# Kernel optimization log

Hardware: AMD Instinct MI355X
Metric: run time of the kernel (lower is better)

The kernel has to match this reference:

```python
import jax, jax.numpy as jnp
import numpy as np

B, C, HZ, WZ, HX, WX = 128, 256, 8, 8, 32, 32
NC = HZ * WZ              # correlation channels = num_channel = 64
TC = max(8, NC // 32)     # CoordAttention bottleneck channels = 8
EPS = 1e-5


def setup_inputs() -> dict:
    key = jax.random.key(0)
    ks = jax.random.split(key, 8)
    z = jax.random.normal(ks[0], (B, C, HZ, WZ), dtype=jnp.float32)
    x = jax.random.normal(ks[1], (B, C, HX, WX), dtype=jnp.float32)
    # 1x1 conv weights stored as [out, in]
    conv1_w = jax.random.normal(ks[2], (TC, NC), dtype=jnp.float32) * (1.0 / np.sqrt(NC))
    conv1_b = jnp.zeros((TC,), dtype=jnp.float32)
    bn_gamma = jnp.ones((TC,), dtype=jnp.float32)
    bn_beta = jnp.zeros((TC,), dtype=jnp.float32)
    conv2_w = jax.random.normal(ks[3], (NC, TC), dtype=jnp.float32) * (1.0 / np.sqrt(TC))
    conv2_b = jnp.zeros((NC,), dtype=jnp.float32)
    conv3_w = jax.random.normal(ks[4], (NC, TC), dtype=jnp.float32) * (1.0 / np.sqrt(TC))
    conv3_b = jnp.zeros((NC,), dtype=jnp.float32)
    return dict(z=z, x=x, conv1_w=conv1_w, conv1_b=conv1_b, bn_gamma=bn_gamma,
                bn_beta=bn_beta, conv2_w=conv2_w, conv2_b=conv2_b,
                conv3_w=conv3_w, conv3_b=conv3_b)


def _h_swish(v):
    return v * jnp.clip(v + 3.0, 0.0, 6.0) / 6.0  # x * relu6(x+3)/6


def reference(z, x, conv1_w, conv1_b, bn_gamma, bn_beta, conv2_w, conv2_b, conv3_w, conv3_b):
    b, c, H, W = x.shape
    # pixel-wise correlation (per-sample loop == batched matmul): [b, Hz*Wz, H, W]
    corr = jnp.einsum('bck,bcn->bkn', z.reshape(b, c, -1), x.reshape(b, c, -1))
    corr = corr.reshape(b, -1, H, W)
    # CoordAttention
    x_h = corr.mean(axis=3)                       # pool over W -> [b, NC, H]
    x_w = corr.mean(axis=2)                       # pool over H -> [b, NC, W]
    x_cat = jnp.concatenate([x_h, x_w], axis=2)   # [b, NC, H+W]
    y = jnp.einsum('oc,bcl->bol', conv1_w, x_cat) + conv1_b[None, :, None]
    # BatchNorm2d (training-mode batch statistics, biased variance)
    mu = y.mean(axis=(0, 2), keepdims=True)
    var = y.var(axis=(0, 2), keepdims=True)
    y = (y - mu) * jax.lax.rsqrt(var + EPS) * bn_gamma[None, :, None] + bn_beta[None, :, None]
    y = _h_swish(y)
    yh, yw = y[:, :, :H], y[:, :, H:]
    out_h = jax.nn.sigmoid(jnp.einsum('oc,bcl->bol', conv2_w, yh) + conv2_b[None, :, None])  # [b, NC, H]
    out_w = jax.nn.sigmoid(jnp.einsum('oc,bcl->bol', conv3_w, yw) + conv3_b[None, :, None])  # [b, NC, W]
    return corr * out_w[:, :, None, :] * out_h[:, :, :, None]
```

## Files before the change

kernel.cpp:

```cpp
#include <hip/hip_runtime.h>
#include <hip/hip_bf16.h>
#include <math.h>

#define B_   128
#define C_   256
#define K_   64
#define N_   1024
#define H_   32
#define W_   32
#define TC_  8
#define L_   64
#define EPS_ 1e-5f

__global__ __launch_bounds__(256) void kA_corr(const float* __restrict__ z,
                                               const float* __restrict__ x,
                                               float* __restrict__ corr,
                                               float* __restrict__ xcat)
{
    __shared__ float zs[64 * 64];
    __shared__ float xs[64 * 64];

    const int t   = blockIdx.x;
    const int b   = blockIdx.y;
    const int tid = threadIdx.x;
    const int tk  = tid & 15;
    const int tn  = tid >> 4;
    const int k0  = tk * 4;
    const int n0  = tn * 4;

    const float* zb = z + (size_t)b * C_ * K_;
    const float* xb = x + (size_t)b * C_ * N_ + t * 64;

    float acc[4][4] = {};

    for (int cc = 0; cc < C_; cc += 64) {
        #pragma unroll
        for (int i = 0; i < 4; ++i) {
            int f4  = tid + i * 256;
            int row = f4 >> 4;
            int col = (f4 & 15) << 2;
            *(float4*)&zs[row * 64 + col] =
                *(const float4*)&zb[(size_t)(cc + row) * K_ + col];
            *(float4*)&xs[row * 64 + col] =
                *(const float4*)&xb[(size_t)(cc + row) * N_ + col];
        }
        __syncthreads();

        #pragma unroll 8
        for (int c = 0; c < 64; ++c) {
            float4 zv = *(float4*)&zs[c * 64 + k0];
            float4 xv = *(float4*)&xs[c * 64 + n0];
            float za[4] = {zv.x, zv.y, zv.z, zv.w};
            float xa[4] = {xv.x, xv.y, xv.z, xv.w};
            #pragma unroll
            for (int i = 0; i < 4; ++i)
                #pragma unroll
                for (int j = 0; j < 4; ++j)
                    acc[i][j] = fmaf(za[i], xa[j], acc[i][j]);
        }
        __syncthreads();
    }

    float* cb = corr + (size_t)b * K_ * N_ + t * 64;
    #pragma unroll
    for (int i = 0; i < 4; ++i) {
        float4 v = make_float4(acc[i][0], acc[i][1], acc[i][2], acc[i][3]);
        *(float4*)&cb[(size_t)(k0 + i) * N_ + n0] = v;
    }

    float* pw = zs;
    float* ph = zs + 2048;

    float rs[4];
    #pragma unroll
    for (int i = 0; i < 4; ++i)
        rs[i] = acc[i][0] + acc[i][1] + acc[i][2] + acc[i][3];
    #pragma unroll
    for (int i = 0; i < 4; ++i)
        ph[(k0 + i) * 16 + tn] = rs[i];

    if (tn < 8) {
        #pragma unroll
        for (int i = 0; i < 4; ++i)
            #pragma unroll
            for (int j = 0; j < 4; ++j)
                pw[(k0 + i) * 32 + n0 + j] = acc[i][j];
    }
    __syncthreads();
    if (tn >= 8) {
        #pragma unroll
        for (int i = 0; i < 4; ++i)
            #pragma unroll
            for (int j = 0; j < 4; ++j)
                pw[(k0 + i) * 32 + (n0 - 32) + j] += acc[i][j];
    }
    __syncthreads();

    float* xcb = xcat + (size_t)b * K_ * L_;
    if (tid < 128) {
        int k = tid >> 1, hl = tid & 1;
        float s = 0.f;
        #pragma unroll
        for (int q = 0; q < 8; ++q) s += ph[k * 16 + hl * 8 + q];
        xcb[k * L_ + 2 * t + hl] = s * (1.f / 32.f);
    }
    #pragma unroll
    for (int r = 0; r < 8; ++r) {
        int idx = tid + r * 256;
        int k = idx >> 5, w = idx & 31;
        atomicAdd(&xcb[k * L_ + 32 + w], pw[k * 32 + w] * (1.f / 32.f));
    }
}

__global__ __launch_bounds__(256) void kB_conv1(const float* __restrict__ xcat,
                                                const float* __restrict__ w1,
                                                const float* __restrict__ b1,
                                                float* __restrict__ ypre,
                                                float* __restrict__ stats)
{
    __shared__ float xc[64 * 64];
    __shared__ float w1s[TC_ * 64];
    __shared__ float ys[TC_ * 64];

    const int b   = blockIdx.x;
    const int tid = threadIdx.x;
    const float* xcb = xcat + (size_t)b * K_ * L_;

    #pragma unroll
    for (int i = 0; i < 4; ++i) {
        int f4 = tid + i * 256;
        *(float4*)&xc[f4 * 4] = *(const float4*)&xcb[f4 * 4];
    }
    if (tid < 128) *(float4*)&w1s[tid * 4] = *(const float4*)&w1[tid * 4];
    __syncthreads();

    const int o0 = tid >> 6;
    const int l  = tid & 63;
    float y0 = 0.f, y1 = 0.f;
    #pragma unroll 8
    for (int k = 0; k < 64; ++k) {
        float xv = xc[k * 64 + l];
        y0 = fmaf(w1s[o0 * 64 + k],        xv, y0);
        y1 = fmaf(w1s[(o0 + 4) * 64 + k],  xv, y1);
    }
    y0 += b1[o0];
    y1 += b1[o0 + 4];
    ypre[((size_t)b * TC_ + o0)     * L_ + l] = y0;
    ypre[((size_t)b * TC_ + o0 + 4) * L_ + l] = y1;
    ys[o0 * L_ + l]       = y0;
    ys[(o0 + 4) * L_ + l] = y1;
    __syncthreads();

    if (tid < TC_) {
        float s = 0.f, sq = 0.f;
        for (int q = 0; q < L_; ++q) {
            float v = ys[tid * L_ + q];
            s += v;
            sq = fmaf(v, v, sq);
        }
        atomicAdd(&stats[tid],       s);
        atomicAdd(&stats[TC_ + tid], sq);
    }
}

__global__ __launch_bounds__(256) void kD_gate(const float* __restrict__ ypre,
                                               const float* __restrict__ stats,
                                               const float* __restrict__ gamma,
                                               const float* __restrict__ beta,
                                               const float* __restrict__ w2,
                                               const float* __restrict__ b2,
                                               const float* __restrict__ w3,
                                               const float* __restrict__ b3,
                                               float* __restrict__ outh,
                                               float* __restrict__ outw)
{
    __shared__ float yn[TC_ * L_];
    __shared__ float w2s[K_ * TC_];
    __shared__ float w3s[K_ * TC_];
    __shared__ float b2s[K_], b3s[K_];

    const int b   = blockIdx.x;
    const int tid = threadIdx.x;
    const float inv_n = 1.f / (float)(B_ * L_);

    #pragma unroll
    for (int r = 0; r < 2; ++r) {
        int idx = tid + r * 256;
        int o   = idx >> 6;
        float mu  = stats[o] * inv_n;
        float var = stats[TC_ + o] * inv_n - mu * mu;
        float v = ypre[(size_t)b * TC_ * L_ + idx];
        v = (v - mu) * (1.f / sqrtf(var + EPS_)) * gamma[o] + beta[o];
        v = v * fminf(fmaxf(v + 3.f, 0.f), 6.f) * (1.f / 6.f);
        yn[idx] = v;
    }
    if (tid < 128)      *(float4*)&w2s[tid * 4]         = *(const float4*)&w2[tid * 4];
    else                *(float4*)&w3s[(tid - 128) * 4] = *(const float4*)&w3[(tid - 128) * 4];
    if (tid < 64)       b2s[tid]       = b2[tid];
    else if (tid < 128) b3s[tid - 64]  = b3[tid - 64];
    __syncthreads();

    #pragma unroll
    for (int r = 0; r < 16; ++r) {
        int idx   = tid + r * 256;
        int which = idx >> 11;
        int o     = (idx >> 5) & 63;
        int p     = idx & 31;
        const float* wsm = which ? w3s : w2s;
        const float* bsm = which ? b3s : b2s;
        float s = bsm[o];
        #pragma unroll
        for (int tt = 0; tt < TC_; ++tt)
            s = fmaf(wsm[o * TC_ + tt], yn[tt * L_ + which * H_ + p], s);
        s = 1.f / (1.f + __expf(-s));
        float* dst = which ? outw : outh;
        dst[((size_t)b * K_ + o) * H_ + p] = s;
    }
}

__global__ __launch_bounds__(256) void kE_final(float* __restrict__ out,
                                                const float* __restrict__ outh,
                                                const float* __restrict__ outw)
{
    int idx = blockIdx.x * 256 + threadIdx.x;
    int w4 = idx & 7;
    int h  = (idx >> 3) & 31;
    int bk = idx >> 8;
    float4 c4 = ((const float4*)out)[idx];
    float  oh = outh[bk * H_ + h];
    float4 ow = *(const float4*)&outw[bk * H_ + w4 * 4];
    c4.x *= ow.x * oh;
    c4.y *= ow.y * oh;
    c4.z *= ow.z * oh;
    c4.w *= ow.w * oh;
    ((float4*)out)[idx] = c4;
}

extern "C" void kernel_launch(void* const* d_in, const int* in_sizes, int n_in,
                              void* d_out, int out_size, void* d_ws, size_t ws_size,
                              hipStream_t stream)
{
    const float* z     = (const float*)d_in[0];
    const float* x     = (const float*)d_in[1];
    const float* w1    = (const float*)d_in[2];
    const float* b1    = (const float*)d_in[3];
    const float* gamma = (const float*)d_in[4];
    const float* beta  = (const float*)d_in[5];
    const float* w2    = (const float*)d_in[6];
    const float* b2    = (const float*)d_in[7];
    const float* w3    = (const float*)d_in[8];
    const float* b3    = (const float*)d_in[9];
    float* out = (float*)d_out;
    float* ws  = (float*)d_ws;

    float* xcat  = ws;
    float* stats = ws + 524288;
    float* ypre  = ws + 524304;
    float* outh  = ws + 589840;
    float* outw  = ws + 852  - 0 + 851984 - 852;
    outw = ws + 851984;

    hipMemsetAsync(ws, 0, (size_t)(524288 + 16) * sizeof(float), stream);

    kA_corr <<<dim3(16, B_), 256, 0, stream>>>(z, x, out, xcat);
    kB_conv1<<<B_,          256, 0, stream>>>(xcat, w1, b1, ypre, stats);
    kD_gate <<<B_,          256, 0, stream>>>(ypre, stats, gamma, beta,
                                              w2, b2, w3, b3, outh, outw);
    kE_final<<<(B_ * K_ * N_) / (256 * 4), 256, 0, stream>>>(out, outh, outw);
}
```

Measured before the change: 268.5 us.

## Retile correlation GEMM to 64x512 blocks with async double-buffered LDS loads

```diff
diff --git a/kernel.cpp b/kernel.cpp
--- a/kernel.cpp
+++ b/kernel.cpp
@@ -12,103 +12,141 @@
 #define L_   64
 #define EPS_ 1e-5f
 
-__global__ __launch_bounds__(256) void kA_corr(const float* __restrict__ z,
-                                               const float* __restrict__ x,
-                                               float* __restrict__ corr,
-                                               float* __restrict__ xcat)
-{
-    __shared__ float zs[64 * 64];
-    __shared__ float xs[64 * 64];
-
-    const int t   = blockIdx.x;
-    const int b   = blockIdx.y;
-    const int tid = threadIdx.x;
-    const int tk  = tid & 15;
-    const int tn  = tid >> 4;
-    const int k0  = tk * 4;
-    const int n0  = tn * 4;
+typedef __attribute__((address_space(3))) void       as3_void;
+typedef const __attribute__((address_space(1))) void as1_void;
+
+__device__ __forceinline__ void gload16(const float* g, float* lds) {
+    __builtin_amdgcn_global_load_lds((as1_void*)g, (as3_void*)lds, 16, 0, 0);
+}
+
+__global__ __launch_bounds__(256, 1) void kA_corr(const float* __restrict__ z,
+                                                  const float* __restrict__ x,
+                                                  float* __restrict__ corr,
+                                                  float* __restrict__ xcat)
+{
+    __shared__ float zs[2][32][64];
+    __shared__ float xs[2][32][512];
+
+    const int nt   = blockIdx.x;
+    const int b    = blockIdx.y;
+    const int tid  = threadIdx.x;
+    const int wv   = tid >> 6;
+    const int lane = tid & 63;
+    const int tk   = tid >> 5;
+    const int tn   = tid & 31;
 
     const float* zb = z + (size_t)b * C_ * K_;
-    const float* xb = x + (size_t)b * C_ * N_ + t * 64;
-
-    float acc[4][4] = {};
-
-    for (int cc = 0; cc < C_; cc += 64) {
-        #pragma unroll
-        for (int i = 0; i < 4; ++i) {
-            int f4  = tid + i * 256;
-            int row = f4 >> 4;
-            int col = (f4 & 15) << 2;
-            *(float4*)&zs[row * 64 + col] =
-                *(const float4*)&zb[(size_t)(cc + row) * K_ + col];
-            *(float4*)&xs[row * 64 + col] =
-                *(const float4*)&xb[(size_t)(cc + row) * N_ + col];
-        }
+    const float* xb = x + (size_t)b * C_ * N_ + nt * 512;
+
+    int sx[4];
+    #pragma unroll
+    for (int r = 0; r < 4; ++r) {
+        int s = tn * 4 + r;
+        sx[r] = s ^ ((s >> 3) & 7);
+    }
+
+    float acc[8][16] = {};
+
+    auto stage = [&](int buf, int cs) {
+        const int cc = cs * 32;
+        #pragma unroll
+        for (int q = 0; q < 18; ++q) {
+            int ch = wv + 4 * q;
+            if (ch < 8) {
+                int row = ch * 4 + (lane >> 4);
+                int col = (lane & 15) * 4;
+                gload16(zb + (size_t)(cc + row) * K_ + col, &zs[buf][ch * 4][0]);
+            } else {
+                int xc  = ch - 8;
+                int qf  = xc * 64 + lane;
+                int row = qf >> 7;
+                int sp  = qf & 127;
+                int sl  = sp ^ ((sp >> 3) & 7);
+                gload16(xb + (size_t)(cc + row) * N_ + sl * 4,
+                        &xs[buf][0][0] + xc * 256);
+            }
+        }
+    };
+
+    stage(0, 0);
+    asm volatile("s_waitcnt vmcnt(0)" ::: "memory");
+    __syncthreads();
+
+    for (int cs = 0; cs < 8; ++cs) {
+        const int cur = cs & 1;
+        if (cs < 7) stage(cur ^ 1, cs + 1);
+
+        #pragma unroll 4
+        for (int c = 0; c < 32; ++c) {
+            const float4* zrow = (const float4*)&zs[cur][c][0];
+            const float4* xrow = (const float4*)&xs[cur][c][0];
+            float4 z0 = zrow[tk * 2];
+            float4 z1 = zrow[tk * 2 + 1];
+            float4 xf0 = xrow[sx[0]];
+            float4 xf1 = xrow[sx[1]];
+            float4 xf2 = xrow[sx[2]];
+            float4 xf3 = xrow[sx[3]];
+            float za[8]  = {z0.x, z0.y, z0.z, z0.w, z1.x, z1.y, z1.z, z1.w};
+            float xa[16] = {xf0.x, xf0.y, xf0.z, xf0.w,
+                            xf1.x, xf1.y, xf1.z, xf1.w,
+                            xf2.x, xf2.y, xf2.z, xf2.w,
+                            xf3.x, xf3.y, xf3.z, xf3.w};
+            #pragma unroll
+            for (int i = 0; i < 8; ++i)
+                #pragma unroll
+                for (int j = 0; j < 16; ++j)
+                    acc[i][j] = fmaf(za[i], xa[j], acc[i][j]);
+        }
+
+        asm volatile("s_waitcnt vmcnt(0)" ::: "memory");
         __syncthreads();
-
-        #pragma unroll 8
-        for (int c = 0; c < 64; ++c) {
-            float4 zv = *(float4*)&zs[c * 64 + k0];
-            float4 xv = *(float4*)&xs[c * 64 + n0];
-            float za[4] = {zv.x, zv.y, zv.z, zv.w};
-            float xa[4] = {xv.x, xv.y, xv.z, xv.w};
-            #pragma unroll
-            for (int i = 0; i < 4; ++i)
-                #pragma unroll
-                for (int j = 0; j < 4; ++j)
-                    acc[i][j] = fmaf(za[i], xa[j], acc[i][j]);
-        }
-        __syncthreads();
-    }
-
-    float* cb = corr + (size_t)b * K_ * N_ + t * 64;
-    #pragma unroll
-    for (int i = 0; i < 4; ++i) {
-        float4 v = make_float4(acc[i][0], acc[i][1], acc[i][2], acc[i][3]);
-        *(float4*)&cb[(size_t)(k0 + i) * N_ + n0] = v;
-    }
-
-    float* pw = zs;
-    float* ph = zs + 2048;
-
-    float rs[4];
-    #pragma unroll
-    for (int i = 0; i < 4; ++i)
-        rs[i] = acc[i][0] + acc[i][1] + acc[i][2] + acc[i][3];
-    #pragma unroll
-    for (int i = 0; i < 4; ++i)
-        ph[(k0 + i) * 16 + tn] = rs[i];
-
-    if (tn < 8) {
-        #pragma unroll
-        for (int i = 0; i < 4; ++i)
-            #pragma unroll
-            for (int j = 0; j < 4; ++j)
-                pw[(k0 + i) * 32 + n0 + j] = acc[i][j];
-    }
-    __syncthreads();
-    if (tn >= 8) {
-        #pragma unroll
-        for (int i = 0; i < 4; ++i)
-            #pragma unroll
-            for (int j = 0; j < 4; ++j)
-                pw[(k0 + i) * 32 + (n0 - 32) + j] += acc[i][j];
+    }
+
+    float* cb = corr + (size_t)b * K_ * N_ + nt * 512;
+    #pragma unroll
+    for (int i = 0; i < 8; ++i) {
+        #pragma unroll
+        for (int r = 0; r < 4; ++r) {
+            float4 v = make_float4(acc[i][4*r], acc[i][4*r+1],
+                                   acc[i][4*r+2], acc[i][4*r+3]);
+            *(float4*)&cb[(size_t)(tk * 8 + i) * N_ + tn * 16 + r * 4] = v;
+        }
+    }
+
+    float (*pwbuf)[64][32] = (float (*)[64][32]) & xs[0][0][0];
+    float (*ph)[32]        = (float (*)[32]) & zs[0][0][0];
+
+    const int hl  = tn >> 1;
+    const int par = tn & 1;
+
+    #pragma unroll
+    for (int i = 0; i < 8; ++i) {
+        float rsum = 0.f;
+        #pragma unroll
+        for (int j = 0; j < 16; ++j) {
+            pwbuf[hl][tk * 8 + i][par * 16 + j] = acc[i][j];
+            rsum += acc[i][j];
+        }
+        ph[tk * 8 + i][tn] = rsum;
     }
     __syncthreads();
 
     float* xcb = xcat + (size_t)b * K_ * L_;
-    if (tid < 128) {
-        int k = tid >> 1, hl = tid & 1;
+    #pragma unroll
+    for (int q = 0; q < 4; ++q) {
+        int idx = tid + q * 256;
+        int k = idx >> 4, hh = idx & 15;
+        float s = ph[k][2 * hh] + ph[k][2 * hh + 1];
+        xcb[k * L_ + nt * 16 + hh] = s * (1.f / 32.f);
+    }
+    #pragma unroll
+    for (int q = 0; q < 8; ++q) {
+        int idx = tid + q * 256;
+        int k = idx >> 5, w = idx & 31;
         float s = 0.f;
         #pragma unroll
-        for (int q = 0; q < 8; ++q) s += ph[k * 16 + hl * 8 + q];
-        xcb[k * L_ + 2 * t + hl] = s * (1.f / 32.f);
-    }
-    #pragma unroll
-    for (int r = 0; r < 8; ++r) {
-        int idx = tid + r * 256;
-        int k = idx >> 5, w = idx & 31;
-        atomicAdd(&xcb[k * L_ + 32 + w], pw[k * 32 + w] * (1.f / 32.f));
+        for (int h2 = 0; h2 < 16; ++h2) s += pwbuf[h2][k][w];
+        atomicAdd(&xcb[k * L_ + 32 + w], s * (1.f / 32.f));
     }
 }
 
@@ -140,8 +178,8 @@
     #pragma unroll 8
     for (int k = 0; k < 64; ++k) {
         float xv = xc[k * 64 + l];
-        y0 = fmaf(w1s[o0 * 64 + k],        xv, y0);
-        y1 = fmaf(w1s[(o0 + 4) * 64 + k],  xv, y1);
+        y0 = fmaf(w1s[o0 * 64 + k],       xv, y0);
+        y1 = fmaf(w1s[(o0 + 4) * 64 + k], xv, y1);
     }
     y0 += b1[o0];
     y1 += b1[o0 + 4];
@@ -196,8 +234,8 @@
     }
     if (tid < 128)      *(float4*)&w2s[tid * 4]         = *(const float4*)&w2[tid * 4];
     else                *(float4*)&w3s[(tid - 128) * 4] = *(const float4*)&w3[(tid - 128) * 4];
-    if (tid < 64)       b2s[tid]       = b2[tid];
-    else if (tid < 128) b3s[tid - 64]  = b3[tid - 64];
+    if (tid < 64)       b2s[tid]      = b2[tid];
+    else if (tid < 128) b3s[tid - 64] = b3[tid - 64];
     __syncthreads();
 
     #pragma unroll
@@ -257,12 +295,11 @@
     float* stats = ws + 524288;
     float* ypre  = ws + 524304;
     float* outh  = ws + 589840;
-    float* outw  = ws + 852  - 0 + 851984 - 852;
-    outw = ws + 851984;
+    float* outw  = ws + 851984;
 
     hipMemsetAsync(ws, 0, (size_t)(524288 + 16) * sizeof(float), stream);
 
-    kA_corr <<<dim3(16, B_), 256, 0, stream>>>(z, x, out, xcat);
+    kA_corr <<<dim3(2, B_), 256, 0, stream>>>(z, x, out, xcat);
     kB_conv1<<<B_,          256, 0, stream>>>(xcat, w1, b1, ypre, stats);
     kD_gate <<<B_,          256, 0, stream>>>(ypre, stats, gamma, beta,
                                               w2, b2, w3, b3, outh, outw);
```

New measurement: 287.1 us. +6.9%, slower.

## Retile correlation GEMM to 64x256 with register prefetch; move pooling to separate kernel

Applied to the files above, without the earlier changes.

```diff
diff --git a/kernel.cpp b/kernel.cpp
--- a/kernel.cpp
+++ b/kernel.cpp
@@ -12,136 +12,142 @@
 #define L_   64
 #define EPS_ 1e-5f
 
-__global__ __launch_bounds__(256) void kA_corr(const float* __restrict__ z,
-                                               const float* __restrict__ x,
-                                               float* __restrict__ corr,
-                                               float* __restrict__ xcat)
-{
-    __shared__ float zs[64 * 64];
-    __shared__ float xs[64 * 64];
-
-    const int t   = blockIdx.x;
+__global__ __launch_bounds__(256, 2) void kA_corr(const float* __restrict__ z,
+                                                  const float* __restrict__ x,
+                                                  float* __restrict__ corr)
+{
+    __shared__ float zs[32][64];
+    __shared__ float xs[32][256];
+
+    const int nt  = blockIdx.x;
     const int b   = blockIdx.y;
     const int tid = threadIdx.x;
-    const int tk  = tid & 15;
-    const int tn  = tid >> 4;
-    const int k0  = tk * 4;
-    const int n0  = tn * 4;
+    const int tk  = tid >> 5;
+    const int tn  = tid & 31;
 
     const float* zb = z + (size_t)b * C_ * K_;
-    const float* xb = x + (size_t)b * C_ * N_ + t * 64;
-
-    float acc[4][4] = {};
-
-    for (int cc = 0; cc < C_; cc += 64) {
-        #pragma unroll
-        for (int i = 0; i < 4; ++i) {
-            int f4  = tid + i * 256;
-            int row = f4 >> 4;
-            int col = (f4 & 15) << 2;
-            *(float4*)&zs[row * 64 + col] =
-                *(const float4*)&zb[(size_t)(cc + row) * K_ + col];
-            *(float4*)&xs[row * 64 + col] =
-                *(const float4*)&xb[(size_t)(cc + row) * N_ + col];
-        }
-        __syncthreads();
+    const float* xb = x + (size_t)b * C_ * N_ + nt * 256;
+
+    const int zrow = tid >> 4;
+    const int zcol = (tid & 15) << 2;
+    const int xrow = tid >> 6;
+    const int sq   = tid & 63;
+    const int sph  = sq ^ ((sq >> 4) & 1);
+
+    const int s0 = (2 * tn) ^ (((2 * tn) >> 4) & 1);
+    const int s1 = (2 * tn + 1) ^ (((2 * tn + 1) >> 4) & 1);
+
+    const float* zg = zb + (size_t)zrow * K_ + zcol;
+    const float* xg = xb + (size_t)xrow * N_ + sq * 4;
+
+    float4 zr[2], xr[8];
+    float  acc[8][8] = {};
+
+    #pragma unroll
+    for (int i = 0; i < 2; ++i) zr[i] = *(const float4*)(zg + (size_t)i * 16 * K_);
+    #pragma unroll
+    for (int i = 0; i < 8; ++i) xr[i] = *(const float4*)(xg + (size_t)i * 4 * N_);
+
+    for (int cs = 0; cs < 8; ++cs) {
+        __syncthreads();
+        #pragma unroll
+        for (int i = 0; i < 2; ++i) *(float4*)&zs[zrow + i * 16][zcol] = zr[i];
+        #pragma unroll
+        for (int i = 0; i < 8; ++i) *(float4*)&xs[xrow + i * 4][sph * 4] = xr[i];
+        __syncthreads();
+
+        if (cs < 7) {
+            const float* zgn = zg + (size_t)(cs + 1) * 32 * K_;
+            const float* xgn = xg + (size_t)(cs + 1) * 32 * N_;
+            #pragma unroll
+            for (int i = 0; i < 2; ++i) zr[i] = *(const float4*)(zgn + (size_t)i * 16 * K_);
+            #pragma unroll
+            for (int i = 0; i < 8; ++i) xr[i] = *(const float4*)(xgn + (size_t)i * 4 * N_);
+        }
 
         #pragma unroll 8
-        for (int c = 0; c < 64; ++c) {
-            float4 zv = *(float4*)&zs[c * 64 + k0];
-            float4 xv = *(float4*)&xs[c * 64 + n0];
-            float za[4] = {zv.x, zv.y, zv.z, zv.w};
-            float xa[4] = {xv.x, xv.y, xv.z, xv.w};
-            #pragma unroll
-            for (int i = 0; i < 4; ++i)
+        for (int c = 0; c < 32; ++c) {
+            float4 z0 = *(float4*)&zs[c][tk * 8];
+            float4 z1 = *(float4*)&zs[c][tk * 8 + 4];
+            float4 x0 = *(float4*)&xs[c][s0 * 4];
+            float4 x1 = *(float4*)&xs[c][s1 * 4];
+            float za[8] = {z0.x, z0.y, z0.z, z0.w, z1.x, z1.y, z1.z, z1.w};
+            float xa[8];
+            xa[0] = x0.x; xa[1] = x0.y; xa[2] = x0.z; xa[3] = x0.w;
+            xa[4] = x1.x; xa[5] = x1.y; xa[6] = x1.z; xa[7] = x1.w;
+            #pragma unroll
+            for (int i = 0; i < 8; ++i)
                 #pragma unroll
-                for (int j = 0; j < 4; ++j)
+                for (int j = 0; j < 8; ++j)
                     acc[i][j] = fmaf(za[i], xa[j], acc[i][j]);
         }
-        __syncthreads();
-    }
-
-    float* cb = corr + (size_t)b * K_ * N_ + t * 64;
-    #pragma unroll
-    for (int i = 0; i < 4; ++i) {
-        float4 v = make_float4(acc[i][0], acc[i][1], acc[i][2], acc[i][3]);
-        *(float4*)&cb[(size_t)(k0 + i) * N_ + n0] = v;
-    }
-
-    float* pw = zs;
-    float* ph = zs + 2048;
-
-    float rs[4];
-    #pragma unroll
-    for (int i = 0; i < 4; ++i)
-        rs[i] = acc[i][0] + acc[i][1] + acc[i][2] + acc[i][3];
-    #pragma unroll
-    for (int i = 0; i < 4; ++i)
-        ph[(k0 + i) * 16 + tn] = rs[i];
-
-    if (tn < 8) {
-        #pragma unroll
-        for (int i = 0; i < 4; ++i)
-            #pragma unroll
-            for (int j = 0; j < 4; ++j)
-                pw[(k0 + i) * 32 + n0 + j] = acc[i][j];
-    }
-    __syncthreads();
-    if (tn >= 8) {
-        #pragma unroll
-        for (int i = 0; i < 4; ++i)
-            #pragma unroll
-            for (int j = 0; j < 4; ++j)
-                pw[(k0 + i) * 32 + (n0 - 32) + j] += acc[i][j];
-    }
-    __syncthreads();
-
-    float* xcb = xcat + (size_t)b * K_ * L_;
-    if (tid < 128) {
-        int k = tid >> 1, hl = tid & 1;
-        float s = 0.f;
-        #pragma unroll
-        for (int q = 0; q < 8; ++q) s += ph[k * 16 + hl * 8 + q];
-        xcb[k * L_ + 2 * t + hl] = s * (1.f / 32.f);
-    }
-    #pragma unroll
-    for (int r = 0; r < 8; ++r) {
-        int idx = tid + r * 256;
-        int k = idx >> 5, w = idx & 31;
-        atomicAdd(&xcb[k * L_ + 32 + w], pw[k * 32 + w] * (1.f / 32.f));
-    }
-}
-
-__global__ __launch_bounds__(256) void kB_conv1(const float* __restrict__ xcat,
-                                                const float* __restrict__ w1,
-                                                const float* __restrict__ b1,
-                                                float* __restrict__ ypre,
-                                                float* __restrict__ stats)
-{
-    __shared__ float xc[64 * 64];
+    }
+
+    float* cb = corr + (size_t)b * K_ * N_ + nt * 256;
+    #pragma unroll
+    for (int i = 0; i < 8; ++i) {
+        float4 lo = make_float4(acc[i][0], acc[i][1], acc[i][2], acc[i][3]);
+        float4 hi = make_float4(acc[i][4], acc[i][5], acc[i][6], acc[i][7]);
+        *(float4*)&cb[(size_t)(tk * 8 + i) * N_ + tn * 8]     = lo;
+        *(float4*)&cb[(size_t)(tk * 8 + i) * N_ + tn * 8 + 4] = hi;
+    }
+}
+
+__global__ __launch_bounds__(256) void kB_pool(const float* __restrict__ corr,
+                                               const float* __restrict__ w1,
+                                               const float* __restrict__ b1,
+                                               float* __restrict__ ypre,
+                                               float* __restrict__ psum)
+{
+    __shared__ float rs[4][1024];
+    __shared__ float xc[64][64];
     __shared__ float w1s[TC_ * 64];
     __shared__ float ys[TC_ * 64];
 
     const int b   = blockIdx.x;
     const int tid = threadIdx.x;
-    const float* xcb = xcat + (size_t)b * K_ * L_;
-
-    #pragma unroll
-    for (int i = 0; i < 4; ++i) {
-        int f4 = tid + i * 256;
-        *(float4*)&xc[f4 * 4] = *(const float4*)&xcb[f4 * 4];
-    }
+    const float* cb = corr + (size_t)b * K_ * N_;
+
     if (tid < 128) *(float4*)&w1s[tid * 4] = *(const float4*)&w1[tid * 4];
-    __syncthreads();
+
+    for (int pass = 0; pass < 16; ++pass) {
+        #pragma unroll
+        for (int i = 0; i < 4; ++i) {
+            int q   = tid + i * 256;
+            int kcl = q >> 8;
+            int off = (q & 255) * 4;
+            *(float4*)&rs[kcl][off] =
+                *(const float4*)&cb[(size_t)(pass * 4 + kcl) * N_ + off];
+        }
+        __syncthreads();
+
+        if (tid < 128) {
+            int kcl = tid >> 5, h = tid & 31;
+            float s = 0.f;
+            #pragma unroll
+            for (int m = 0; m < 8; ++m) {
+                float4 v = *(float4*)&rs[kcl][h * 32 + (((m + h) & 7) << 2)];
+                s += v.x + v.y + v.z + v.w;
+            }
+            xc[pass * 4 + kcl][h] = s * (1.f / 32.f);
+        } else {
+            int kcl = (tid - 128) >> 5, w = (tid - 128) & 31;
+            float s = 0.f;
+            #pragma unroll
+            for (int h2 = 0; h2 < 32; ++h2) s += rs[kcl][h2 * 32 + w];
+            xc[pass * 4 + kcl][32 + w] = s * (1.f / 32.f);
+        }
+        __syncthreads();
+    }
 
     const int o0 = tid >> 6;
     const int l  = tid & 63;
     float y0 = 0.f, y1 = 0.f;
     #pragma unroll 8
     for (int k = 0; k < 64; ++k) {
-        float xv = xc[k * 64 + l];
-        y0 = fmaf(w1s[o0 * 64 + k],        xv, y0);
-        y1 = fmaf(w1s[(o0 + 4) * 64 + k],  xv, y1);
+        float xv = xc[k][l];
+        y0 = fmaf(w1s[o0 * 64 + k],       xv, y0);
+        y1 = fmaf(w1s[(o0 + 4) * 64 + k], xv, y1);
     }
     y0 += b1[o0];
     y1 += b1[o0 + 4];
@@ -153,18 +159,19 @@
 
     if (tid < TC_) {
         float s = 0.f, sq = 0.f;
-        for (int q = 0; q < L_; ++q) {
-            float v = ys[tid * L_ + q];
-            s += v;
-            sq = fmaf(v, v, sq);
-        }
-        atomicAdd(&stats[tid],       s);
-        atomicAdd(&stats[TC_ + tid], sq);
+        #pragma unroll
+        for (int m = 0; m < 16; ++m) {
+            float4 v = *(float4*)&ys[tid * 64 + m * 4];
+            s  += v.x + v.y + v.z + v.w;
+            sq += v.x * v.x + v.y * v.y + v.z * v.z + v.w * v.w;
+        }
+        psum[b * 16 + tid]       = s;
+        psum[b * 16 + 8 + tid]   = sq;
     }
 }
 
 __global__ __launch_bounds__(256) void kD_gate(const float* __restrict__ ypre,
-                                               const float* __restrict__ stats,
+                                               const float* __restrict__ psum,
                                                const float* __restrict__ gamma,
                                                const float* __restrict__ beta,
                                                const float* __restrict__ w2,
@@ -174,6 +181,8 @@
                                                float* __restrict__ outh,
                                                float* __restrict__ outw)
 {
+    __shared__ float sred[16][17];
+    __shared__ float stats[16];
     __shared__ float yn[TC_ * L_];
     __shared__ float w2s[K_ * TC_];
     __shared__ float w3s[K_ * TC_];
@@ -181,14 +190,29 @@
 
     const int b   = blockIdx.x;
     const int tid = threadIdx.x;
+
+    {
+        float p = 0.f;
+        #pragma unroll
+        for (int m = 0; m < 8; ++m) p += psum[tid + 256 * m];
+        sred[tid & 15][tid >> 4] = p;
+    }
+    __syncthreads();
+    if (tid < 16) {
+        float s = 0.f;
+        #pragma unroll
+        for (int c = 0; c < 16; ++c) s += sred[tid][c];
+        stats[tid] = s;
+    }
+    __syncthreads();
+
     const float inv_n = 1.f / (float)(B_ * L_);
-
     #pragma unroll
     for (int r = 0; r < 2; ++r) {
         int idx = tid + r * 256;
         int o   = idx >> 6;
         float mu  = stats[o] * inv_n;
-        float var = stats[TC_ + o] * inv_n - mu * mu;
+        float var = stats[8 + o] * inv_n - mu * mu;
         float v = ypre[(size_t)b * TC_ * L_ + idx];
         v = (v - mu) * (1.f / sqrtf(var + EPS_)) * gamma[o] + beta[o];
         v = v * fminf(fmaxf(v + 3.f, 0.f), 6.f) * (1.f / 6.f);
@@ -196,8 +220,8 @@
     }
     if (tid < 128)      *(float4*)&w2s[tid * 4]         = *(const float4*)&w2[tid * 4];
     else                *(float4*)&w3s[(tid - 128) * 4] = *(const float4*)&w3[(tid - 128) * 4];
-    if (tid < 64)       b2s[tid]       = b2[tid];
-    else if (tid < 128) b3s[tid - 64]  = b3[tid - 64];
+    if (tid < 64)       b2s[tid]      = b2[tid];
+    else if (tid < 128) b3s[tid - 64] = b3[tid - 64];
     __syncthreads();
 
     #pragma unroll
@@ -253,18 +277,14 @@
     float* out = (float*)d_out;
     float* ws  = (float*)d_ws;
 
-    float* xcat  = ws;
-    float* stats = ws + 524288;
-    float* ypre  = ws + 524304;
-    float* outh  = ws + 589840;
-    float* outw  = ws + 852  - 0 + 851984 - 852;
-    outw = ws + 851984;
-
-    hipMemsetAsync(ws, 0, (size_t)(524288 + 16) * sizeof(float), stream);
-
-    kA_corr <<<dim3(16, B_), 256, 0, stream>>>(z, x, out, xcat);
-    kB_conv1<<<B_,          256, 0, stream>>>(xcat, w1, b1, ypre, stats);
-    kD_gate <<<B_,          256, 0, stream>>>(ypre, stats, gamma, beta,
+    float* ypre = ws;
+    float* psum = ws + 65536;
+    float* outh = ws + 67584;
+    float* outw = ws + 329728;
+
+    kA_corr <<<dim3(4, B_), 256, 0, stream>>>(z, x, out);
+    kB_pool <<<B_,          256, 0, stream>>>(out, w1, b1, ypre, psum);
+    kD_gate <<<B_,          256, 0, stream>>>(ypre, psum, gamma, beta,
                                               w2, b2, w3, b3, outh, outw);
     kE_final<<<(B_ * K_ * N_) / (256 * 4), 256, 0, stream>>>(out, outh, outw);
 }
```

Measured after the change: 301.0 us. 12.1% more time.
